# Kernel optimization log

Hardware: AMD Instinct MI355X
Metric: run time of the kernel (lower is better)

The kernel has to match this reference:

```python
import jax, jax.numpy as jnp
import numpy as np

NGRID, NLAYER = 8192, 24
NPERIODS, NOBS, NC = 50, 4096, 200
SIGMA = 1.0
VREF = 3.0          # reference crustal Vs (km/s) for depth-sensitivity scale
RAYLEIGH_FACTOR = 0.92


def setup_inputs() -> dict:
    key = jax.random.key(0)
    k1, k2, k3 = jax.random.split(key, 3)
    # S-wave velocity model, 2.0-4.0 km/s, flattened as in log_prob(Vs_flat)
    Vs_flat = (2.0 + 2.0 * jax.random.uniform(k1, (NGRID, NLAYER))).reshape(-1).astype(jnp.float32)
    # Ray-path averaging matrix: nonnegative, rows sum to 1 (slowness average)
    A = jax.random.uniform(k2, (NOBS, NGRID), dtype=jnp.float32)
    A = A / A.sum(axis=1, keepdims=True)
    # Beamforming energy spectra per observation pair: (Nobs, Nperiods, Nc)
    energy = jax.random.uniform(k3, (NOBS, NPERIODS, NC), dtype=jnp.float32)
    # Monotone phase-velocity axis per observation: (Nobs, Nc)
    c_axis = jnp.zeros((NOBS, NC), jnp.float32) + jnp.linspace(1.5, 5.0, NC, dtype=jnp.float32)
    thick = jnp.full((NLAYER,), 2.0, jnp.float32)          # 2 km layers
    periods = jnp.linspace(1.0, 60.0, NPERIODS, dtype=jnp.float32)
    return {"Vs_flat": Vs_flat, "A": A, "energy": energy, "c_axis": c_axis,
            "thick": thick, "periods": periods}


def _dispersion_all_cells(Vs, thick, periods):
    # Differentiable surrogate for the batched surf96 forward across all grid cells.
    # Vs: (G, L), thick: (L,), periods: (P,)  ->  c_true: (G, P)
    z = jnp.cumsum(thick) - 0.5 * thick                      # layer-center depths (L,)
    depth_scale = VREF * periods / 3.0                       # ~ sensing depth per period (P,)
    w = jnp.exp(-z[None, :] / depth_scale[:, None]) * thick[None, :]  # (P, L)
    w = w / w.sum(axis=1, keepdims=True)
    return RAYLEIGH_FACTOR * jnp.einsum('pl,gl->gp', w, Vs)  # (G, P)


def reference(Vs_flat, A, energy, c_axis, thick, periods):
    Vs = Vs_flat.reshape(NGRID, NLAYER)
    c_true = _dispersion_all_cells(Vs, thick, periods)       # (Ngrid, Nperiods)
    # _apply_A: slowness averaging along ray paths
    s_pred = A @ (1.0 / c_true)                              # (Nobs, Nperiods)
    c_pred = 1.0 / s_pred
    # _interp1d_torch, vectorized over all (obs, period) pairs
    idx = jax.vmap(jnp.searchsorted)(c_axis, c_pred)         # (Nobs, Nperiods)
    idx = jnp.clip(idx, 1, NC - 1)
    c0 = jnp.take_along_axis(c_axis, idx - 1, axis=1)
    c1 = jnp.take_along_axis(c_axis, idx, axis=1)
    e0 = jnp.take_along_axis(energy, (idx - 1)[:, :, None], axis=2)[..., 0]
    e1 = jnp.take_along_axis(energy, idx[:, :, None], axis=2)[..., 0]
    w = (c_pred - c0) / (c1 - c0 + 1e-12)
    e_interp = e0 + w * (e1 - e0)
    e_max = energy.max(axis=-1)                              # (Nobs, Nperiods)
    log_like = -jnp.sum(e_max - e_interp) / (SIGMA ** 2)
    return log_like
```

## Files before the change

kernel.cpp:

```cpp
#include <hip/hip_runtime.h>

#define NGRID 8192
#define NLAYER 24
#define NPERIODS 50
#define NOBS 4096
#define NC 200
#define PP 64
#define NSPLIT 16
#define SPLITG (NGRID / NSPLIT)
#define WPB 4
#define GC (SPLITG / WPB)
#define KG 16
#define ASTR 20
#define DOT 128
#define NBINS 1024
#define VREF 3.0f
#define K2LDSF (WPB * DOT * ASTR)

__global__ __launch_bounds__(256) void k1_rpad(const float* __restrict__ Vs,
                                               const float* __restrict__ thick,
                                               const float* __restrict__ periods,
                                               float* __restrict__ r_pad,
                                               float* __restrict__ bins) {
    __shared__ float w_sh[NLAYER][NPERIODS];
    __shared__ float z_sh[NLAYER];
    int tid = threadIdx.x;
    if (blockIdx.x == 0) {
        for (int i = tid; i < NBINS; i += 256) bins[i] = 0.f;
    }
    if (tid < NLAYER) {
        float c = 0.f;
        for (int i = 0; i <= tid; ++i) c += thick[i];
        z_sh[tid] = c - 0.5f * thick[tid];
    }
    __syncthreads();
    if (tid < NPERIODS) {
        float ds = (VREF / 3.0f) * periods[tid];
        float tmp[NLAYER];
        float s = 0.f;
        #pragma unroll
        for (int l = 0; l < NLAYER; ++l) {
            float v = expf(-z_sh[l] / ds) * thick[l];
            tmp[l] = v; s += v;
        }
        float inv = 1.f / s;
        #pragma unroll
        for (int l = 0; l < NLAYER; ++l) w_sh[l][tid] = tmp[l] * inv;
    }
    __syncthreads();
    int idx = blockIdx.x * 256 + tid;
    int g = idx >> 6, p = idx & 63;
    float r = 0.f;
    if (p < NPERIODS) {
        const float4* vp = (const float4*)(Vs + (size_t)g * NLAYER);
        float s = 0.f;
        #pragma unroll
        for (int q = 0; q < NLAYER / 4; ++q) {
            float4 t = vp[q];
            s = fmaf(w_sh[4*q+0][p], t.x, s);
            s = fmaf(w_sh[4*q+1][p], t.y, s);
            s = fmaf(w_sh[4*q+2][p], t.z, s);
            s = fmaf(w_sh[4*q+3][p], t.w, s);
        }
        r = 1.0f / (0.92f * s);
    }
    r_pad[idx] = r;
}

__global__ __launch_bounds__(256) void k2_gemm(const float* __restrict__ A,
                                               const float* __restrict__ r_pad,
                                               float* __restrict__ partial) {
    __shared__ float lds[K2LDSF];
    int tid  = threadIdx.x;
    int lane = tid & 63;
    int wv   = __builtin_amdgcn_readfirstlane(tid >> 6);
    int o_base = blockIdx.x * DOT;
    int split  = blockIdx.y;
    float* Aw = lds + wv * (DOT * ASTR);

    float acc0[NPERIODS], acc1[NPERIODS];
    #pragma unroll
    for (int p = 0; p < NPERIODS; ++p) { acc0[p] = 0.f; acc1[p] = 0.f; }

    int g_wave = split * SPLITG + wv * GC;

    #pragma unroll 1
    for (int kt = 0; kt < GC / KG; ++kt) {
        int g0 = g_wave + kt * KG;
        #pragma unroll
        for (int s = 0; s < 8; ++s) {
            int f   = s * 64 + lane;
            int row = f >> 2;
            int c4  = (f & 3) * 4;
            float4 t = *(const float4*)(A + (size_t)(o_base + row) * NGRID + g0 + c4);
            *(float4*)(Aw + row * ASTR + c4) = t;
        }
        #pragma unroll 1
        for (int gg = 0; gg < KG; gg += 4) {
            float4 a0 = *(const float4*)(Aw + lane * ASTR + gg);
            float4 a1 = *(const float4*)(Aw + (64 + lane) * ASTR + gg);
            const float* rr = r_pad + (size_t)(g0 + gg) * PP;
            #pragma unroll
            for (int j = 0; j < 4; ++j) {
                float aj0 = (j == 0) ? a0.x : (j == 1) ? a0.y : (j == 2) ? a0.z : a0.w;
                float aj1 = (j == 0) ? a1.x : (j == 1) ? a1.y : (j == 2) ? a1.z : a1.w;
                const float* rj = rr + j * PP;
                #pragma unroll
                for (int p = 0; p < NPERIODS; ++p) {
                    float rv = rj[p];
                    acc0[p] = fmaf(aj0, rv, acc0[p]);
                    acc1[p] = fmaf(aj1, rv, acc1[p]);
                }
            }
        }
    }

    float* outp = partial + (size_t)split * (NOBS * NPERIODS) + (size_t)o_base * NPERIODS;
    #pragma unroll
    for (int h = 0; h < 4; ++h) {
        __syncthreads();
        float* rw = lds + wv * (DOT * 17);
        #pragma unroll
        for (int q = 0; q < 16; ++q) {
            int p = h * 16 + q;
            rw[lane * 17 + q]        = (p < NPERIODS) ? acc0[p] : 0.f;
            rw[(64 + lane) * 17 + q] = (p < NPERIODS) ? acc1[p] : 0.f;
        }
        __syncthreads();
        for (int e = tid; e < DOT * 16; e += 256) {
            int oo = e >> 4, q = e & 15;
            int p  = h * 16 + q;
            if (p < NPERIODS) {
                float v = 0.f;
                #pragma unroll
                for (int w2 = 0; w2 < WPB; ++w2) v += lds[w2 * (DOT * 17) + oo * 17 + q];
                outp[oo * NPERIODS + p] = v;
            }
        }
    }
}

__global__ __launch_bounds__(256) void k3_main(const float* __restrict__ energy,
                                               const float* __restrict__ c_axis,
                                               const float* __restrict__ partial,
                                               float* __restrict__ bins) {
    __shared__ float csh[NC];
    __shared__ float cp_sh[64];
    __shared__ float red[4];
    int tid  = threadIdx.x;
    int lane = tid & 63;
    int wv   = tid >> 6;
    int o    = blockIdx.x;

    if (tid < NC) csh[tid] = c_axis[(size_t)o * NC + tid];
    if (tid >= 192) {
        int p = tid - 192;
        float v = 0.f;
        if (p < NPERIODS) {
            float s = 0.f;
            #pragma unroll
            for (int sp = 0; sp < NSPLIT; ++sp)
                s += partial[(size_t)sp * (NOBS * NPERIODS) + (size_t)o * NPERIODS + p];
            v = 1.0f / s;
        }
        cp_sh[p] = v;
    }
    __syncthreads();

    bool act = lane < NC / 4;
    float4 ca = act ? *(const float4*)(csh + 4 * lane) : make_float4(9e30f, 9e30f, 9e30f, 9e30f);
    const float* ebase = energy + (size_t)o * NPERIODS * NC;
    float local = 0.f;

    for (int p0 = wv; p0 < NPERIODS; p0 += 8) {
        int p1 = p0 + 4;
        bool has1 = p1 < NPERIODS;
        int p1c = has1 ? p1 : p0;
        float cpA = cp_sh[p0];
        float cpB = cp_sh[p1c];
        const float* erA = ebase + (size_t)p0 * NC;
        const float* erB = ebase + (size_t)p1c * NC;
        float4 eA = act ? *(const float4*)(erA + 4 * lane) : make_float4(-1e30f, -1e30f, -1e30f, -1e30f);
        float4 eB = act ? *(const float4*)(erB + 4 * lane) : make_float4(-1e30f, -1e30f, -1e30f, -1e30f);

        int cntA = __popcll(__ballot(ca.x < cpA)) + __popcll(__ballot(ca.y < cpA))
                 + __popcll(__ballot(ca.z < cpA)) + __popcll(__ballot(ca.w < cpA));
        int cntB = __popcll(__ballot(ca.x < cpB)) + __popcll(__ballot(ca.y < cpB))
                 + __popcll(__ballot(ca.z < cpB)) + __popcll(__ballot(ca.w < cpB));

        float mA = fmaxf(fmaxf(eA.x, eA.y), fmaxf(eA.z, eA.w));
        float mB = fmaxf(fmaxf(eB.x, eB.y), fmaxf(eB.z, eB.w));
        #pragma unroll
        for (int m = 32; m; m >>= 1) {
            mA = fmaxf(mA, __shfl_xor(mA, m, 64));
            mB = fmaxf(mB, __shfl_xor(mB, m, 64));
        }

        int iA = cntA < 1 ? 1 : (cntA > NC - 1 ? NC - 1 : cntA);
        int iB = cntB < 1 ? 1 : (cntB > NC - 1 ? NC - 1 : cntB);

        int a0 = iA - 1, a1 = iA, b0 = iB - 1, b1 = iB;
        float sA0 = ((a0 & 3) == 0) ? eA.x : ((a0 & 3) == 1) ? eA.y : ((a0 & 3) == 2) ? eA.z : eA.w;
        float sA1 = ((a1 & 3) == 0) ? eA.x : ((a1 & 3) == 1) ? eA.y : ((a1 & 3) == 2) ? eA.z : eA.w;
        float sB0 = ((b0 & 3) == 0) ? eB.x : ((b0 & 3) == 1) ? eB.y : ((b0 & 3) == 2) ? eB.z : eB.w;
        float sB1 = ((b1 & 3) == 0) ? eB.x : ((b1 & 3) == 1) ? eB.y : ((b1 & 3) == 2) ? eB.z : eB.w;
        float e0A = __shfl(sA0, a0 >> 2, 64), e1A = __shfl(sA1, a1 >> 2, 64);
        float e0B = __shfl(sB0, b0 >> 2, 64), e1B = __shfl(sB1, b1 >> 2, 64);

        float c0A = csh[a0], c1A = csh[a1];
        float c0B = csh[b0], c1B = csh[b1];
        float wA = (cpA - c0A) / (c1A - c0A + 1e-12f);
        float wB = (cpB - c0B) / (c1B - c0B + 1e-12f);
        float eiA = fmaf(wA, e1A - e0A, e0A);
        float eiB = fmaf(wB, e1B - e0B, e0B);
        local += mA - eiA;
        local += has1 ? (mB - eiB) : 0.f;
    }
    if (lane == 0) red[wv] = local;
    __syncthreads();
    if (tid == 0)
        atomicAdd(&bins[blockIdx.x & (NBINS - 1)], red[0] + red[1] + red[2] + red[3]);
}

__global__ __launch_bounds__(256) void k4_final(const float* __restrict__ bins,
                                                float* __restrict__ out) {
    __shared__ float red[4];
    int tid = threadIdx.x;
    float s = 0.f;
    for (int i = tid; i < NBINS; i += 256) s += bins[i];
    #pragma unroll
    for (int m = 32; m; m >>= 1) s += __shfl_xor(s, m, 64);
    int lane = tid & 63, wv = tid >> 6;
    if (lane == 0) red[wv] = s;
    __syncthreads();
    if (tid == 0) out[0] = -(red[0] + red[1] + red[2] + red[3]);
}

extern "C" void kernel_launch(void* const* d_in, const int* in_sizes, int n_in,
                              void* d_out, int out_size, void* d_ws, size_t ws_size,
                              hipStream_t stream) {
    const float* Vs      = (const float*)d_in[0];
    const float* A       = (const float*)d_in[1];
    const float* energy  = (const float*)d_in[2];
    const float* c_axis  = (const float*)d_in[3];
    const float* thick   = (const float*)d_in[4];
    const float* periods = (const float*)d_in[5];
    float* out = (float*)d_out;

    float* ws      = (float*)d_ws;
    float* r_pad   = ws;
    float* partial = r_pad + (size_t)NGRID * PP;
    float* bins    = partial + (size_t)NSPLIT * NOBS * NPERIODS;

    hipLaunchKernelGGL(k1_rpad, dim3((NGRID * 64) / 256), dim3(256), 0, stream,
                       Vs, thick, periods, r_pad, bins);
    hipLaunchKernelGGL(k2_gemm, dim3(NOBS / DOT, NSPLIT), dim3(256), 0, stream,
                       A, r_pad, partial);
    hipLaunchKernelGGL(k3_main, dim3(NOBS), dim3(256), 0, stream,
                       energy, c_axis, partial, bins);
    hipLaunchKernelGGL(k4_final, dim3(1), dim3(256), 0, stream, bins, out);
}
```

Before: 371.7 us.

## Prefetch A and r tiles into registers and stage r through LDS

Software-pipelines the GEMM inner loop. The next K-tile of A and r_pad is loaded into registers while the current tile is consumed from LDS. r values are now staged per wave in LDS and read as float4 broadcasts instead of wave-uniform global loads. This aims to hide global load latency, at the cost of extra VGPRs and LDS traffic, which may reduce occupancy or replace cheap scalar-cache reads.

Measured after the change: 404.8 us. 8.9% more time.

```diff
diff --git a/kernel.cpp b/kernel.cpp
--- a/kernel.cpp
+++ b/kernel.cpp
@@ -12,10 +12,12 @@
 #define GC (SPLITG / WPB)
 #define KG 16
 #define ASTR 20
+#define RSTR 64
 #define DOT 128
 #define NBINS 1024
 #define VREF 3.0f
-#define K2LDSF (WPB * DOT * ASTR)
+#define WLDSF (DOT * ASTR + KG * RSTR)
+#define K2LDSF (WPB * WLDSF)
 
 __global__ __launch_bounds__(256) void k1_rpad(const float* __restrict__ Vs,
                                                const float* __restrict__ thick,
@@ -76,41 +78,72 @@
     int wv   = __builtin_amdgcn_readfirstlane(tid >> 6);
     int o_base = blockIdx.x * DOT;
     int split  = blockIdx.y;
-    float* Aw = lds + wv * (DOT * ASTR);
+    float* Aw = lds + wv * WLDSF;
+    float* Rw = Aw + DOT * ASTR;
 
     float acc0[NPERIODS], acc1[NPERIODS];
     #pragma unroll
     for (int p = 0; p < NPERIODS; ++p) { acc0[p] = 0.f; acc1[p] = 0.f; }
 
     int g_wave = split * SPLITG + wv * GC;
+
+    float4 aS[8], rS[4];
+    #pragma unroll
+    for (int s = 0; s < 8; ++s)
+        aS[s] = *(const float4*)(A + (size_t)(o_base + s * 16 + (lane >> 2)) * NGRID
+                                 + g_wave + (lane & 3) * 4);
+    #pragma unroll
+    for (int s = 0; s < 4; ++s)
+        rS[s] = *(const float4*)(r_pad + (size_t)(g_wave + s * 4 + (lane >> 4)) * PP
+                                 + (lane & 15) * 4);
 
     #pragma unroll 1
     for (int kt = 0; kt < GC / KG; ++kt) {
-        int g0 = g_wave + kt * KG;
-        #pragma unroll
-        for (int s = 0; s < 8; ++s) {
-            int f   = s * 64 + lane;
-            int row = f >> 2;
-            int c4  = (f & 3) * 4;
-            float4 t = *(const float4*)(A + (size_t)(o_base + row) * NGRID + g0 + c4);
-            *(float4*)(Aw + row * ASTR + c4) = t;
-        }
+        #pragma unroll
+        for (int s = 0; s < 8; ++s)
+            *(float4*)(Aw + (s * 16 + (lane >> 2)) * ASTR + (lane & 3) * 4) = aS[s];
+        #pragma unroll
+        for (int s = 0; s < 4; ++s)
+            *(float4*)(Rw + (s * 64 + lane) * 4) = rS[s];
+
+        if (kt + 1 < GC / KG) {
+            int gn = g_wave + (kt + 1) * KG;
+            #pragma unroll
+            for (int s = 0; s < 8; ++s)
+                aS[s] = *(const float4*)(A + (size_t)(o_base + s * 16 + (lane >> 2)) * NGRID
+                                         + gn + (lane & 3) * 4);
+            #pragma unroll
+            for (int s = 0; s < 4; ++s)
+                rS[s] = *(const float4*)(r_pad + (size_t)(gn + s * 4 + (lane >> 4)) * PP
+                                         + (lane & 15) * 4);
+        }
+
         #pragma unroll 1
         for (int gg = 0; gg < KG; gg += 4) {
             float4 a0 = *(const float4*)(Aw + lane * ASTR + gg);
             float4 a1 = *(const float4*)(Aw + (64 + lane) * ASTR + gg);
-            const float* rr = r_pad + (size_t)(g0 + gg) * PP;
             #pragma unroll
             for (int j = 0; j < 4; ++j) {
                 float aj0 = (j == 0) ? a0.x : (j == 1) ? a0.y : (j == 2) ? a0.z : a0.w;
                 float aj1 = (j == 0) ? a1.x : (j == 1) ? a1.y : (j == 2) ? a1.z : a1.w;
-                const float* rj = rr + j * PP;
+                const float* rj = Rw + (gg + j) * RSTR;
                 #pragma unroll
-                for (int p = 0; p < NPERIODS; ++p) {
-                    float rv = rj[p];
-                    acc0[p] = fmaf(aj0, rv, acc0[p]);
-                    acc1[p] = fmaf(aj1, rv, acc1[p]);
+                for (int q = 0; q < 12; ++q) {
+                    float4 rv = *(const float4*)(rj + 4 * q);
+                    acc0[4*q+0] = fmaf(aj0, rv.x, acc0[4*q+0]);
+                    acc0[4*q+1] = fmaf(aj0, rv.y, acc0[4*q+1]);
+                    acc0[4*q+2] = fmaf(aj0, rv.z, acc0[4*q+2]);
+                    acc0[4*q+3] = fmaf(aj0, rv.w, acc0[4*q+3]);
+                    acc1[4*q+0] = fmaf(aj1, rv.x, acc1[4*q+0]);
+                    acc1[4*q+1] = fmaf(aj1, rv.y, acc1[4*q+1]);
+                    acc1[4*q+2] = fmaf(aj1, rv.z, acc1[4*q+2]);
+                    acc1[4*q+3] = fmaf(aj1, rv.w, acc1[4*q+3]);
                 }
+                float2 rv2 = *(const float2*)(rj + 48);
+                acc0[48] = fmaf(aj0, rv2.x, acc0[48]);
+                acc0[49] = fmaf(aj0, rv2.y, acc0[49]);
+                acc1[48] = fmaf(aj1, rv2.x, acc1[48]);
+                acc1[49] = fmaf(aj1, rv2.y, acc1[49]);
             }
         }
     }
```
